# Performance work log

Measured on AMD Instinct MI355X. Metric: run time of the kernel, lower is better.

Reference implementation:

```python
import jax, jax.numpy as jnp
import numpy as np
import math

INPUT_SIZE = 20
HIDDEN = 1500
OUTPUT = 20
MLP_HID = math.ceil(5 / 4 * HIDDEN)  # 1875
T = 4096


def setup_inputs() -> dict:
    key = jax.random.key(0)
    ks = jax.random.split(key, 10)
    s_lstm = 1.0 / np.sqrt(HIDDEN)
    s1 = 1.0 / np.sqrt(HIDDEN)
    s2 = 1.0 / np.sqrt(MLP_HID)
    return {
        "input_seq": jax.random.normal(ks[0], (T, INPUT_SIZE), dtype=jnp.float32),
        "W_ih": jax.random.uniform(ks[1], (4 * HIDDEN, INPUT_SIZE), jnp.float32, -s_lstm, s_lstm),
        "W_hh": jax.random.uniform(ks[2], (4 * HIDDEN, HIDDEN), jnp.float32, -s_lstm, s_lstm),
        "b_ih": jax.random.uniform(ks[3], (4 * HIDDEN,), jnp.float32, -s_lstm, s_lstm),
        "b_hh": jax.random.uniform(ks[4], (4 * HIDDEN,), jnp.float32, -s_lstm, s_lstm),
        "W1": jax.random.uniform(ks[5], (MLP_HID, HIDDEN), jnp.float32, -s1, s1),
        "b1": jax.random.uniform(ks[6], (MLP_HID,), jnp.float32, -s1, s1),
        "W2": jax.random.uniform(ks[7], (OUTPUT, MLP_HID), jnp.float32, -s2, s2),
        "b2": jax.random.uniform(ks[8], (OUTPUT,), jnp.float32, -s2, s2),
    }


def reference(input_seq, W_ih, W_hh, b_ih, b_hh, W1, b1, W2, b2):
    H = W_hh.shape[1]
    # Precompute input contribution for all timesteps: (T, 4H)
    x_proj = input_seq @ W_ih.T + (b_ih + b_hh)

    def step(carry, xp):
        h, c = carry
        gates = xp + h @ W_hh.T  # (4H,)
        i, f, g, o = jnp.split(gates, 4)
        i = jax.nn.sigmoid(i)
        f = jax.nn.sigmoid(f)
        g = jnp.tanh(g)
        o = jax.nn.sigmoid(o)
        c_new = f * c + i * g
        h_new = o * jnp.tanh(c_new)
        return (h_new, c_new), None

    h0 = jnp.zeros((H,), dtype=input_seq.dtype)
    c0 = jnp.zeros((H,), dtype=input_seq.dtype)
    (h_last, _), _ = jax.lax.scan(step, (h0, c0), x_proj)
    # Dropout is identity in eval mode. Module returns predictions[-1],
    # which only depends on the last hidden state.
    hid = h_last @ W1.T + b1
    return hid @ W2.T + b2
```

## Files before the change

kernel.cpp:

```cpp
#include <hip/hip_runtime.h>
#include <math.h>

#define TT 4096
#define HH 1500
#define NB 250
#define NT 512
#define NREP 8

typedef unsigned uv4 __attribute__((ext_vector_type(4)));
typedef _Float16 h2f __attribute__((ext_vector_type(2)));
typedef _Float16 h4f __attribute__((ext_vector_type(4)));

#define ALD4(p)   __hip_atomic_load((p), __ATOMIC_RELAXED, __HIP_MEMORY_SCOPE_AGENT)
#define AST4(p,v) __hip_atomic_store((p), (v), __ATOMIC_RELAXED, __HIP_MEMORY_SCOPE_AGENT)

__device__ __forceinline__ float fast_sigmoid(float z) {
  return 1.0f / (1.0f + __expf(-z));
}
__device__ __forceinline__ float fast_tanh(float z) {
  float az = fabsf(z);
  float e  = __expf(-2.0f * az);
  float r  = (1.0f - e) / (1.0f + e);
  return copysignf(r, z);
}
__device__ __forceinline__ float dot2(unsigned wb, unsigned hb, float acc) {
#if __has_builtin(__builtin_amdgcn_fdot2)
  return __builtin_amdgcn_fdot2(__builtin_bit_cast(h2f, wb),
                                __builtin_bit_cast(h2f, hb), acc, false);
#else
  h2f w = __builtin_bit_cast(h2f, wb), h = __builtin_bit_cast(h2f, hb);
  acc = fmaf((float)w.x, (float)h.x, acc);
  return fmaf((float)w.y, (float)h.y, acc);
#endif
}

__device__ __forceinline__ void poll3(const unsigned* a0, const unsigned* a1,
                                      const unsigned* a2,
                                      uv4& v0, uv4& v1, uv4& v2) {
  asm volatile(
      "global_load_dwordx4 %0, %3, off sc0 sc1\n\t"
      "global_load_dwordx4 %1, %4, off sc0 sc1\n\t"
      "global_load_dwordx4 %2, %5, off sc0 sc1\n\t"
      "s_waitcnt vmcnt(0)"
      : "=&v"(v0), "=&v"(v1), "=&v"(v2)
      : "v"(a0), "v"(a1), "v"(a2)
      : "memory");
}
__device__ __forceinline__ h4f cvt4h(uv4 v) {
  h4f r;
  r.x = (_Float16)__uint_as_float(v.x);
  r.y = (_Float16)__uint_as_float(v.y);
  r.z = (_Float16)__uint_as_float(v.z);
  r.w = (_Float16)__uint_as_float(v.w);
  return r;
}

__global__
__attribute__((amdgpu_flat_work_group_size(NT, NT), amdgpu_waves_per_eu(2, 2)))
void lstm_fused(
    const float* __restrict__ x,
    const float* __restrict__ Wih,
    const float* __restrict__ Whh,
    const float* __restrict__ bih,
    const float* __restrict__ bhh,
    const float* __restrict__ W1,
    const float* __restrict__ b1,
    const float* __restrict__ W2,
    const float* __restrict__ b2,
    float* __restrict__ out,
    unsigned* __restrict__ ws)
{
  const int tid = threadIdx.x;
  const int bid = blockIdx.x;
  const int wv  = tid >> 6;
  const int ln  = tid & 63;

  unsigned* pub  = ws;
  unsigned* hidp = ws + NREP * 2 * 1536;

  __shared__ __align__(16) _Float16 lds_wh[24 * 1536];
  __shared__ __align__(16) _Float16 lds_hh[1536];
  __shared__ __align__(16) float    lds_hf[1536];
  __shared__ float lds_xp[2][24];
  __shared__ float lds_gs[4][6];
  float* lds_hd = (float*)lds_wh;

  for (int hi = tid; hi < 24 * 1536; hi += NT) {
    const int r = hi / 1536, k = hi - r * 1536;
    const int u = r >> 2, g = r & 3;
    const size_t grow = (size_t)(g * HH + bid * 6 + u) * HH;
    const float v = (k < HH) ? Whh[grow + k] : 0.f;
    lds_wh[hi] = (_Float16)v;
  }

  const int uu = (wv < 6) ? wv : 0;
  const uv4* wp = ((const uv4*)lds_wh) + (size_t)uu * 4 * 192;
  const uv4* hp = (const uv4*)lds_hh;

  float4 wx0, wx1, wx2, wx3, wx4;
  float4 xr0, xr1, xr2, xr3, xr4;
  float bias = 0.f;
  if (wv == 6 && ln < 24) {
    const int g = ln / 6, u = ln - g * 6;
    const int row = g * HH + bid * 6 + u;
    const float4* s = (const float4*)(Wih + row * 20);
    wx0 = s[0]; wx1 = s[1]; wx2 = s[2]; wx3 = s[3]; wx4 = s[4];
    bias = bih[row] + bhh[row];
    const float4* xx = (const float4*)x;
    xr0 = xx[0]; xr1 = xx[1]; xr2 = xx[2]; xr3 = xx[3]; xr4 = xx[4];
  }

  float c = 0.f;

  if (tid < 6 * NREP)
    AST4(pub + (tid / 6) * 3072 + 6 * bid + (tid % 6), 1u);

  __syncthreads();

  unsigned* myrep = pub + (bid & (NREP - 1)) * 3072;

  for (int t = 0; t < TT; ++t) {
    const int s = t & 1;
    const unsigned tag = (unsigned)((t + 1) & 15);

    uv4 pw[12];
    if (wv < 6) {
      #pragma unroll
      for (int g = 0; g < 4; ++g) {
        #pragma unroll
        for (int m = 0; m < 3; ++m) pw[g * 3 + m] = wp[g * 192 + ln + 64 * m];
      }
    } else {
      if (wv == 6 && ln < 24) {
        float sx = bias;
        sx += wx0.x*xr0.x + wx0.y*xr0.y + wx0.z*xr0.z + wx0.w*xr0.w;
        sx += wx1.x*xr1.x + wx1.y*xr1.y + wx1.z*xr1.z + wx1.w*xr1.w;
        sx += wx2.x*xr2.x + wx2.y*xr2.y + wx2.z*xr2.z + wx2.w*xr2.w;
        sx += wx3.x*xr3.x + wx3.y*xr3.y + wx3.z*xr3.z + wx3.w*xr3.w;
        sx += wx4.x*xr4.x + wx4.y*xr4.y + wx4.z*xr4.z + wx4.w*xr4.w;
        lds_xp[s][ln] = sx;
      }
      const int p4 = (tid - 384) << 2;
      unsigned* base = myrep + s * 1536;
      uv4 v0, v1, v2;
      for (;;) {
        poll3(base + p4, base + p4 + 512, base + p4 + 1024, v0, v1, v2);
        unsigned miss = ((v0.x & 15u) ^ tag) | ((v0.y & 15u) ^ tag)
                      | ((v0.z & 15u) ^ tag) | ((v0.w & 15u) ^ tag)
                      | ((v1.x & 15u) ^ tag) | ((v1.y & 15u) ^ tag)
                      | ((v1.z & 15u) ^ tag) | ((v1.w & 15u) ^ tag);
        if (p4 + 1024 < HH)
          miss |= ((v2.x & 15u) ^ tag) | ((v2.y & 15u) ^ tag)
                | ((v2.z & 15u) ^ tag) | ((v2.w & 15u) ^ tag);
        if (!__any(miss != 0u)) break;
        __builtin_amdgcn_s_sleep(1);
      }
      *(h4f*)(lds_hh + p4)       = cvt4h(v0);
      *(h4f*)(lds_hh + p4 + 512) = cvt4h(v1);
      h4f z = {(_Float16)0.f, (_Float16)0.f, (_Float16)0.f, (_Float16)0.f};
      *(h4f*)(lds_hh + p4 + 1024) = (p4 + 1024 < HH) ? cvt4h(v2) : z;
    }
    __syncthreads();

    if (wv < 6) {
      uv4 hv[3];
      #pragma unroll
      for (int m = 0; m < 3; ++m) hv[m] = hp[ln + 64 * m];
      float a[4] = {0.f, 0.f, 0.f, 0.f};
      #pragma unroll
      for (int g = 0; g < 4; ++g) {
        #pragma unroll
        for (int m = 0; m < 3; ++m) {
          const uv4 q = pw[g * 3 + m], h = hv[m];
          a[g] = dot2(q.x, h.x, a[g]);
          a[g] = dot2(q.y, h.y, a[g]);
          a[g] = dot2(q.z, h.z, a[g]);
          a[g] = dot2(q.w, h.w, a[g]);
        }
      }
      #pragma unroll
      for (int g = 0; g < 4; ++g) {
        a[g] += __shfl_xor(a[g], 16, 64);
        a[g] += __shfl_xor(a[g], 32, 64);
      }
      const int q4 = ln >> 4;
      float v = (q4 == 0) ? a[0] : (q4 == 1) ? a[1] : (q4 == 2) ? a[2] : a[3];
      v += __shfl_xor(v, 1, 64);
      v += __shfl_xor(v, 2, 64);
      v += __shfl_xor(v, 4, 64);
      v += __shfl_xor(v, 8, 64);
      if ((ln & 15) == 0) lds_gs[q4][wv] = v;
    } else if (wv == 6 && ln < 24 && (t + 1) < TT) {
      const float4* xx = (const float4*)(x + 20 * (t + 1));
      xr0 = xx[0]; xr1 = xx[1]; xr2 = xx[2]; xr3 = xx[3]; xr4 = xx[4];
    }
    __syncthreads();

    if (wv == 7) {
      unsigned bits = 0u;
      if (ln < 6) {
        const int u = ln;
        const float zi = lds_gs[0][u] + lds_xp[s][0 + u];
        const float zf = lds_gs[1][u] + lds_xp[s][6 + u];
        const float zg = lds_gs[2][u] + lds_xp[s][12 + u];
        const float zo = lds_gs[3][u] + lds_xp[s][18 + u];
        const float ig = fast_sigmoid(zi);
        const float fg = fast_sigmoid(zf);
        const float gg = fast_tanh(zg);
        const float og = fast_sigmoid(zo);
        c = fg * c + ig * gg;
        const float hn = og * fast_tanh(c);
        bits = (__float_as_uint(hn) & ~15u) | (unsigned)((t + 2) & 15);
      }
      const int u6 = ln % 6;
      const unsigned myb = (unsigned)__shfl((int)bits, u6, 64);
      if (ln < 6 * NREP) {
        const int rep = ln / 6;
        AST4(pub + rep * 3072 + ((t + 1) & 1) * 1536 + 6 * bid + u6, myb);
      }
    }
  }

  if (wv >= 6) {
    const unsigned tagf = (unsigned)((TT + 1) & 15);
    const int p4 = (tid - 384) << 2;
    unsigned* base = myrep;
    uv4 v0, v1, v2;
    for (;;) {
      poll3(base + p4, base + p4 + 512, base + p4 + 1024, v0, v1, v2);
      unsigned miss = ((v0.x & 15u) ^ tagf) | ((v0.y & 15u) ^ tagf)
                    | ((v0.z & 15u) ^ tagf) | ((v0.w & 15u) ^ tagf)
                    | ((v1.x & 15u) ^ tagf) | ((v1.y & 15u) ^ tagf)
                    | ((v1.z & 15u) ^ tagf) | ((v1.w & 15u) ^ tagf);
      if (p4 + 1024 < HH)
        miss |= ((v2.x & 15u) ^ tagf) | ((v2.y & 15u) ^ tagf)
              | ((v2.z & 15u) ^ tagf) | ((v2.w & 15u) ^ tagf);
      if (!__any(miss != 0u)) break;
      __builtin_amdgcn_s_sleep(1);
    }
    float4 f0 = {__uint_as_float(v0.x), __uint_as_float(v0.y),
                 __uint_as_float(v0.z), __uint_as_float(v0.w)};
    float4 f1 = {__uint_as_float(v1.x), __uint_as_float(v1.y),
                 __uint_as_float(v1.z), __uint_as_float(v1.w)};
    float4 f2 = {__uint_as_float(v2.x), __uint_as_float(v2.y),
                 __uint_as_float(v2.z), __uint_as_float(v2.w)};
    float4 z4 = {0.f, 0.f, 0.f, 0.f};
    *(float4*)(lds_hf + p4)        = f0;
    *(float4*)(lds_hf + p4 + 512)  = f1;
    *(float4*)(lds_hf + p4 + 1024) = (p4 + 1024 < HH) ? f2 : z4;
  }
  __syncthreads();

  {
    const float4* h4 = (const float4*)lds_hf;
    const int r = bid + 250 * wv;
    if (r < 1875) {
      const float4* wrow = (const float4*)(W1 + (size_t)r * HH);
      float ss = 0.f;
      #pragma unroll
      for (int m = 0; m < 6; ++m) {
        const int idx = ln + 64 * m;
        if (idx < 375) {
          const float4 a = wrow[idx], hv = h4[idx];
          ss += a.x*hv.x + a.y*hv.y + a.z*hv.z + a.w*hv.w;
        }
      }
      #pragma unroll
      for (int off = 32; off > 0; off >>= 1) ss += __shfl_xor(ss, off, 64);
      if (ln == 0) {
        const float vv = ss + b1[r];
        AST4(hidp + r, (__float_as_uint(vv) & ~15u) | 5u);
      }
    }
  }
  if (bid != 0) return;

  __syncthreads();
  for (int j = tid; j < 1875; j += NT) {
    unsigned bts;
    for (;;) {
      bts = ALD4(hidp + j);
      if ((bts & 15u) == 5u) break;
      __builtin_amdgcn_s_sleep(1);
    }
    lds_hd[j] = __uint_as_float(bts);
  }
  __syncthreads();

  for (int r = wv; r < 20; r += 8) {
    float ss = 0.f;
    for (int k = ln; k < 1875; k += 64)
      ss = fmaf(W2[(size_t)r * 1875 + k], lds_hd[k], ss);
    #pragma unroll
    for (int off = 32; off > 0; off >>= 1) ss += __shfl_xor(ss, off, 64);
    if (ln == 0) out[r] = ss + b2[r];
  }
}

extern "C" void kernel_launch(void* const* d_in, const int* in_sizes, int n_in,
                              void* d_out, int out_size, void* d_ws, size_t ws_size,
                              hipStream_t stream) {
  const float* x   = (const float*)d_in[0];
  const float* Wih = (const float*)d_in[1];
  const float* Whh = (const float*)d_in[2];
  const float* bih = (const float*)d_in[3];
  const float* bhh = (const float*)d_in[4];
  const float* W1  = (const float*)d_in[5];
  const float* b1  = (const float*)d_in[6];
  const float* W2  = (const float*)d_in[7];
  const float* b2  = (const float*)d_in[8];
  float* out   = (float*)d_out;
  unsigned* ws = (unsigned*)d_ws;

  hipLaunchKernelGGL(lstm_fused, dim3(NB), dim3(NT), 0, stream,
                     x, Wih, Whh, bih, bhh, W1, b1, W2, b2, out, ws);
}
```

Before: 10.70 ms.

## Halve persistent LSTM block count, giving each block twelve hidden units

Cuts the persistent grid from 250 to 125 blocks. Each block now holds 12 hidden units' W_hh rows in LDS, and each compute wave does two unit dot products per step. Publishing uses 64-bit stores, and the final hidden-state poll and the MLP row loop are reworked to fit the new block count. The aim is to lower cross-block synchronisation and polling traffic per timestep, at the cost of doubled per-wave compute, more registers and more LDS per block.

```diff
diff --git a/kernel.cpp b/kernel.cpp
--- a/kernel.cpp
+++ b/kernel.cpp
@@ -3,7 +3,7 @@
 
 #define TT 4096
 #define HH 1500
-#define NB 250
+#define NB 125
 #define NT 512
 #define NREP 8
 
@@ -13,6 +13,7 @@
 
 #define ALD4(p)   __hip_atomic_load((p), __ATOMIC_RELAXED, __HIP_MEMORY_SCOPE_AGENT)
 #define AST4(p,v) __hip_atomic_store((p), (v), __ATOMIC_RELAXED, __HIP_MEMORY_SCOPE_AGENT)
+#define AST8(p,v) __hip_atomic_store((p), (v), __ATOMIC_RELAXED, __HIP_MEMORY_SCOPE_AGENT)
 
 __device__ __forceinline__ float fast_sigmoid(float z) {
   return 1.0f / (1.0f + __expf(-z));
@@ -78,33 +79,34 @@
   unsigned* pub  = ws;
   unsigned* hidp = ws + NREP * 2 * 1536;
 
-  __shared__ __align__(16) _Float16 lds_wh[24 * 1536];
+  __shared__ __align__(16) _Float16 lds_wh[48 * 1536];
   __shared__ __align__(16) _Float16 lds_hh[1536];
   __shared__ __align__(16) float    lds_hf[1536];
-  __shared__ float lds_xp[2][24];
-  __shared__ float lds_gs[4][6];
+  __shared__ float lds_xp[2][48];
+  __shared__ float lds_gs[4][12];
   float* lds_hd = (float*)lds_wh;
 
-  for (int hi = tid; hi < 24 * 1536; hi += NT) {
+  for (int hi = tid; hi < 48 * 1536; hi += NT) {
     const int r = hi / 1536, k = hi - r * 1536;
     const int u = r >> 2, g = r & 3;
-    const size_t grow = (size_t)(g * HH + bid * 6 + u) * HH;
+    const size_t grow = (size_t)(g * HH + bid * 12 + u) * HH;
     const float v = (k < HH) ? Whh[grow + k] : 0.f;
     lds_wh[hi] = (_Float16)v;
   }
 
   const int uu = (wv < 6) ? wv : 0;
-  const uv4* wp = ((const uv4*)lds_wh) + (size_t)uu * 4 * 192;
+  const uv4* wpA = ((const uv4*)lds_wh) + (size_t)(2 * uu) * 4 * 192;
+  const uv4* wpB = wpA + 4 * 192;
   const uv4* hp = (const uv4*)lds_hh;
 
   float4 wx0, wx1, wx2, wx3, wx4;
   float4 xr0, xr1, xr2, xr3, xr4;
   float bias = 0.f;
-  if (wv == 6 && ln < 24) {
-    const int g = ln / 6, u = ln - g * 6;
-    const int row = g * HH + bid * 6 + u;
-    const float4* s = (const float4*)(Wih + row * 20);
-    wx0 = s[0]; wx1 = s[1]; wx2 = s[2]; wx3 = s[3]; wx4 = s[4];
+  if (wv == 6 && ln < 48) {
+    const int g = ln / 12, u = ln - g * 12;
+    const int row = g * HH + bid * 12 + u;
+    const float4* sp = (const float4*)(Wih + row * 20);
+    wx0 = sp[0]; wx1 = sp[1]; wx2 = sp[2]; wx3 = sp[3]; wx4 = sp[4];
     bias = bih[row] + bhh[row];
     const float4* xx = (const float4*)x;
     xr0 = xx[0]; xr1 = xx[1]; xr2 = xx[2]; xr3 = xx[3]; xr4 = xx[4];
@@ -112,8 +114,8 @@
 
   float c = 0.f;
 
-  if (tid < 6 * NREP)
-    AST4(pub + (tid / 6) * 3072 + 6 * bid + (tid % 6), 1u);
+  if (tid < 12 * NREP)
+    AST4(pub + (tid / 12) * 3072 + 12 * bid + (tid % 12), 1u);
 
   __syncthreads();
 
@@ -123,15 +125,18 @@
     const int s = t & 1;
     const unsigned tag = (unsigned)((t + 1) & 15);
 
-    uv4 pw[12];
+    uv4 pw[24];
     if (wv < 6) {
       #pragma unroll
       for (int g = 0; g < 4; ++g) {
         #pragma unroll
-        for (int m = 0; m < 3; ++m) pw[g * 3 + m] = wp[g * 192 + ln + 64 * m];
+        for (int m = 0; m < 3; ++m) {
+          pw[g * 3 + m]      = wpA[g * 192 + ln + 64 * m];
+          pw[12 + g * 3 + m] = wpB[g * 192 + ln + 64 * m];
+        }
       }
     } else {
-      if (wv == 6 && ln < 24) {
+      if (wv == 6 && ln < 48) {
         float sx = bias;
         sx += wx0.x*xr0.x + wx0.y*xr0.y + wx0.z*xr0.z + wx0.w*xr0.w;
         sx += wx1.x*xr1.x + wx1.y*xr1.y + wx1.z*xr1.z + wx1.w*xr1.w;
@@ -166,31 +171,45 @@
       uv4 hv[3];
       #pragma unroll
       for (int m = 0; m < 3; ++m) hv[m] = hp[ln + 64 * m];
-      float a[4] = {0.f, 0.f, 0.f, 0.f};
+      float a0[4] = {0.f, 0.f, 0.f, 0.f};
+      float a1[4] = {0.f, 0.f, 0.f, 0.f};
       #pragma unroll
       for (int g = 0; g < 4; ++g) {
         #pragma unroll
         for (int m = 0; m < 3; ++m) {
-          const uv4 q = pw[g * 3 + m], h = hv[m];
-          a[g] = dot2(q.x, h.x, a[g]);
-          a[g] = dot2(q.y, h.y, a[g]);
-          a[g] = dot2(q.z, h.z, a[g]);
-          a[g] = dot2(q.w, h.w, a[g]);
+          const uv4 h = hv[m];
+          const uv4 qa = pw[g * 3 + m];
+          a0[g] = dot2(qa.x, h.x, a0[g]);
+          a0[g] = dot2(qa.y, h.y, a0[g]);
+          a0[g] = dot2(qa.z, h.z, a0[g]);
+          a0[g] = dot2(qa.w, h.w, a0[g]);
+          const uv4 qb = pw[12 + g * 3 + m];
+          a1[g] = dot2(qb.x, h.x, a1[g]);
+          a1[g] = dot2(qb.y, h.y, a1[g]);
+          a1[g] = dot2(qb.z, h.z, a1[g]);
+          a1[g] = dot2(qb.w, h.w, a1[g]);
         }
       }
       #pragma unroll
       for (int g = 0; g < 4; ++g) {
-        a[g] += __shfl_xor(a[g], 16, 64);
-        a[g] += __shfl_xor(a[g], 32, 64);
+        a0[g] += __shfl_xor(a0[g], 16, 64);
+        a0[g] += __shfl_xor(a0[g], 32, 64);
+        a1[g] += __shfl_xor(a1[g], 16, 64);
+        a1[g] += __shfl_xor(a1[g], 32, 64);
       }
       const int q4 = ln >> 4;
-      float v = (q4 == 0) ? a[0] : (q4 == 1) ? a[1] : (q4 == 2) ? a[2] : a[3];
-      v += __shfl_xor(v, 1, 64);
-      v += __shfl_xor(v, 2, 64);
-      v += __shfl_xor(v, 4, 64);
-      v += __shfl_xor(v, 8, 64);
-      if ((ln & 15) == 0) lds_gs[q4][wv] = v;
-    } else if (wv == 6 && ln < 24 && (t + 1) < TT) {
+      float v0 = (q4 == 0) ? a0[0] : (q4 == 1) ? a0[1] : (q4 == 2) ? a0[2] : a0[3];
+      float v1 = (q4 == 0) ? a1[0] : (q4 == 1) ? a1[1] : (q4 == 2) ? a1[2] : a1[3];
+      #pragma unroll
+      for (int off = 1; off <= 8; off <<= 1) {
+        v0 += __shfl_xor(v0, off, 64);
+        v1 += __shfl_xor(v1, off, 64);
+      }
+      if ((ln & 15) == 0) {
+        lds_gs[q4][2 * wv]     = v0;
+        lds_gs[q4][2 * wv + 1] = v1;
+      }
+    } else if (wv == 6 && ln < 48 && (t + 1) < TT) {
       const float4* xx = (const float4*)(x + 20 * (t + 1));
       xr0 = xx[0]; xr1 = xx[1]; xr2 = xx[2]; xr3 = xx[3]; xr4 = xx[4];
     }
@@ -198,12 +217,12 @@
 
     if (wv == 7) {
       unsigned bits = 0u;
-      if (ln < 6) {
+      if (ln < 12) {
         const int u = ln;
         const float zi = lds_gs[0][u] + lds_xp[s][0 + u];
-        const float zf = lds_gs[1][u] + lds_xp[s][6 + u];
-        const float zg = lds_gs[2][u] + lds_xp[s][12 + u];
-        const float zo = lds_gs[3][u] + lds_xp[s][18 + u];
+        const float zf = lds_gs[1][u] + lds_xp[s][12 + u];
+        const float zg = lds_gs[2][u] + lds_xp[s][24 + u];
+        const float zo = lds_gs[3][u] + lds_xp[s][36 + u];
         const float ig = fast_sigmoid(zi);
         const float fg = fast_sigmoid(zf);
         const float gg = fast_tanh(zg);
@@ -212,49 +231,47 @@
         const float hn = og * fast_tanh(c);
         bits = (__float_as_uint(hn) & ~15u) | (unsigned)((t + 2) & 15);
       }
-      const int u6 = ln % 6;
-      const unsigned myb = (unsigned)__shfl((int)bits, u6, 64);
-      if (ln < 6 * NREP) {
+      const int m6 = ln % 6;
+      const unsigned d0 = (unsigned)__shfl((int)bits, 2 * m6, 64);
+      const unsigned d1 = (unsigned)__shfl((int)bits, 2 * m6 + 1, 64);
+      if (ln < 48) {
         const int rep = ln / 6;
-        AST4(pub + rep * 3072 + ((t + 1) & 1) * 1536 + 6 * bid + u6, myb);
-      }
-    }
-  }
-
-  if (wv >= 6) {
+        const unsigned long long dd =
+            (unsigned long long)d0 | ((unsigned long long)d1 << 32);
+        AST8((unsigned long long*)(pub + rep * 3072 + ((t + 1) & 1) * 1536 +
+                                   12 * bid + 2 * m6), dd);
+      }
+    }
+  }
+
+  {
     const unsigned tagf = (unsigned)((TT + 1) & 15);
-    const int p4 = (tid - 384) << 2;
-    unsigned* base = myrep;
-    uv4 v0, v1, v2;
-    for (;;) {
-      poll3(base + p4, base + p4 + 512, base + p4 + 1024, v0, v1, v2);
-      unsigned miss = ((v0.x & 15u) ^ tagf) | ((v0.y & 15u) ^ tagf)
-                    | ((v0.z & 15u) ^ tagf) | ((v0.w & 15u) ^ tagf)
-                    | ((v1.x & 15u) ^ tagf) | ((v1.y & 15u) ^ tagf)
-                    | ((v1.z & 15u) ^ tagf) | ((v1.w & 15u) ^ tagf);
-      if (p4 + 1024 < HH)
-        miss |= ((v2.x & 15u) ^ tagf) | ((v2.y & 15u) ^ tagf)
-              | ((v2.z & 15u) ^ tagf) | ((v2.w & 15u) ^ tagf);
-      if (!__any(miss != 0u)) break;
-      __builtin_amdgcn_s_sleep(1);
-    }
-    float4 f0 = {__uint_as_float(v0.x), __uint_as_float(v0.y),
-                 __uint_as_float(v0.z), __uint_as_float(v0.w)};
-    float4 f1 = {__uint_as_float(v1.x), __uint_as_float(v1.y),
-                 __uint_as_float(v1.z), __uint_as_float(v1.w)};
-    float4 f2 = {__uint_as_float(v2.x), __uint_as_float(v2.y),
-                 __uint_as_float(v2.z), __uint_as_float(v2.w)};
-    float4 z4 = {0.f, 0.f, 0.f, 0.f};
-    *(float4*)(lds_hf + p4)        = f0;
-    *(float4*)(lds_hf + p4 + 512)  = f1;
-    *(float4*)(lds_hf + p4 + 1024) = (p4 + 1024 < HH) ? f2 : z4;
+    if (tid < 375) {
+      const unsigned* ap = myrep + (tid << 2);
+      uv4 v;
+      for (;;) {
+        asm volatile("global_load_dwordx4 %0, %1, off sc0 sc1\n\t"
+                     "s_waitcnt vmcnt(0)"
+                     : "=&v"(v) : "v"(ap) : "memory");
+        const unsigned miss = ((v.x & 15u) ^ tagf) | ((v.y & 15u) ^ tagf)
+                            | ((v.z & 15u) ^ tagf) | ((v.w & 15u) ^ tagf);
+        if (!miss) break;
+        __builtin_amdgcn_s_sleep(1);
+      }
+      float4 f = {__uint_as_float(v.x), __uint_as_float(v.y),
+                  __uint_as_float(v.z), __uint_as_float(v.w)};
+      *(float4*)(lds_hf + (tid << 2)) = f;
+    } else if (tid < 384) {
+      float4 z4 = {0.f, 0.f, 0.f, 0.f};
+      *(float4*)(lds_hf + (tid << 2)) = z4;
+    }
   }
   __syncthreads();
 
   {
     const float4* h4 = (const float4*)lds_hf;
-    const int r = bid + 250 * wv;
-    if (r < 1875) {
+    for (int k = wv; k < 15; k += 8) {
+      const int r = bid + NB * k;
       const float4* wrow = (const float4*)(W1 + (size_t)r * HH);
       float ss = 0.f;
       #pragma unroll
```

Result: faster. 10.25 ms, median of 2 (-4.2%).
